# Performance work log

Hardware: AMD Instinct MI355X
Metric: run time of the kernel (lower is better)

The kernel has to match this reference:

```python
import jax, jax.numpy as jnp
import numpy as np

S = 8192; HID = 2048; H = 16; D = 128; BLK = 256; NC = S // BLK
GROUPS = 8; EPS = 1e-5; ROPE_THETA = 600000.0
LAYER_ID = 0; NLAYERS = 20
SCALE = D ** -0.5

def _build_slopes():
    # ALiBi-style slopes (H is a power of 2), scaled by layer decay factor
    start = 2.0 ** (-2.0 ** (-(np.log2(H) - 3.0)))
    slopes = np.array([start * start ** i for i in range(H)], dtype=np.float32)
    return slopes * np.float32(1.0 - LAYER_ID / (NLAYERS - 1) + 1e-5)

SLOPES = jnp.asarray(_build_slopes())  # [H]

def _rmsnorm(x, w, eps=EPS):
    return x * jax.lax.rsqrt(jnp.mean(x * x, axis=-1, keepdims=True) + eps) * w

def _rope(x, positions):
    # neox-style rotary, x: [S, H, D]
    half = D // 2
    inv_freq = 1.0 / (ROPE_THETA ** (jnp.arange(0, D, 2, dtype=jnp.float32) / D))
    freqs = positions.astype(jnp.float32)[:, None] * inv_freq  # [S, half]
    cos = jnp.cos(freqs)[:, None, :]
    sin = jnp.sin(freqs)[:, None, :]
    x1, x2 = x[..., :half], x[..., half:]
    return jnp.concatenate([x1 * cos - x2 * sin, x2 * cos + x1 * sin], axis=-1)

def _lightning_attn(q, k, v):
    # chunked recurrent linear attention with per-head exponential decay
    # q,k,v: [S, H, D] fp32 -> [S, H*D]
    qc = q.reshape(NC, BLK, H, D).transpose(0, 2, 1, 3)  # [NC, H, BLK, D]
    kc = k.reshape(NC, BLK, H, D).transpose(0, 2, 1, 3)
    vc = v.reshape(NC, BLK, H, D).transpose(0, 2, 1, 3)
    idx = jnp.arange(BLK, dtype=jnp.float32)
    q_decay = jnp.exp(-SLOPES[:, None, None] * (idx + 1.0)[None, :, None])       # [H,BLK,1]
    k_decay = jnp.exp(-SLOPES[:, None, None] * (BLK - 1.0 - idx)[None, :, None])  # [H,BLK,1]
    blk_decay = jnp.exp(-SLOPES * BLK)[:, None, None]                             # [H,1,1]
    dif = idx[:, None] - idx[None, :]
    causal = dif >= 0
    diag_decay = jnp.where(causal, jnp.exp(-SLOPES[:, None, None] * jnp.where(causal, dif, 0.0)), 0.0)  # [H,BLK,BLK]

    def step(kv, inp):
        qb, kb, vb = inp  # each [H, BLK, D]
        qk = jnp.einsum('hid,hjd->hij', qb, kb) * diag_decay
        intra = jnp.einsum('hij,hjd->hid', qk, vb)
        inter = jnp.einsum('hid,hde->hie', qb * q_decay, kv)
        kv_new = blk_decay * kv + jnp.einsum('hjd,hje->hde', kb * k_decay, vb)
        return kv_new, intra + inter

    kv0 = jnp.zeros((H, D, D), dtype=jnp.float32)
    _, out = jax.lax.scan(step, kv0, (qc, kc, vc))  # out: [NC, H, BLK, D]
    return out.transpose(0, 2, 1, 3).reshape(S, H * D)

def setup_inputs() -> dict:
    key = jax.random.key(0)
    ks = jax.random.split(key, 6)
    return {
        'hidden_states': jax.random.normal(ks[0], (S, HID), jnp.float32),
        'positions': jnp.arange(S, dtype=jnp.int32),
        'qkv_w': jax.random.normal(ks[1], (3 * H * D, HID), jnp.float32) * 0.02,
        'qkv_b': jax.random.normal(ks[2], (3 * H * D,), jnp.float32) * 0.01,
        'q_norm_w': jnp.ones((D,), jnp.float32),
        'k_norm_w': jnp.ones((D,), jnp.float32),
        'g_w': jax.random.normal(ks[3], (H * D, HID), jnp.float32) * 0.02,
        'g_norm_w': jnp.ones((H * D,), jnp.float32),
        'dense_w': jax.random.normal(ks[4], (HID, H * D), jnp.float32) * 0.02,
    }

def reference(hidden_states, positions, qkv_w, qkv_b, q_norm_w, k_norm_w, g_w, g_norm_w, dense_w):
    hs = hidden_states.astype(jnp.float32)
    qkv = hs @ qkv_w.T + qkv_b                      # [S, 3*H*D], fp32 (linear_silu=False)
    q, k, v = jnp.split(qkv, [H * D, 2 * H * D], axis=-1)
    q = q.reshape(S, H, D); k = k.reshape(S, H, D); v = v.reshape(S, H, D)
    q = _rmsnorm(q, q_norm_w)                       # use_qk_norm per-head RMSNorm
    k = _rmsnorm(k, k_norm_w)
    q = _rope(q, positions)                         # linear_rope=True
    k = _rope(k, positions)
    q = q * SCALE                                   # linear_scale (minimax backend)
    attn = _lightning_attn(q, k, v)                 # [S, H*D]
    g = hs @ g_w.T                                  # output gate
    xg = attn.reshape(S, GROUPS, (H * D) // GROUPS)  # group RMSNorm (norm_before_gate)
    rstd = jax.lax.rsqrt(jnp.mean(xg * xg, axis=-1, keepdims=True) + EPS)
    y = (xg * rstd).reshape(S, H * D) * g_norm_w * jax.nn.sigmoid(g)
    return y @ dense_w.T                            # [S, HID]
```

## Files before the change

### kernel.cpp

```cpp
#include <hip/hip_runtime.h>

#define S_LEN 8192
#define HID   2048
#define NH    16
#define HD    128
#define BLKC  256
#define QKV_STRIDE 6144
#define EPSV  1e-5f
#define SCALEF 0.08838834764831845f

typedef unsigned short u16;
typedef unsigned int   u32;
typedef __attribute__((ext_vector_type(8))) short bf16x8;
typedef __attribute__((ext_vector_type(4))) float f32x4;

__device__ __forceinline__ float b2f(u16 u) {
    unsigned int x = ((unsigned int)u) << 16;
    return __uint_as_float(x);
}
__device__ __forceinline__ u16 f2b(float f) {
    unsigned int u = __float_as_uint(f);
    u += 0x7fff + ((u >> 16) & 1);
    return (u16)(u >> 16);
}
__device__ __forceinline__ u32 pack2(float lo, float hi) {
    return (u32)f2b(lo) | ((u32)f2b(hi) << 16);
}
__device__ __forceinline__ float get_slope(int h) {
    return exp2f(-0.5f * (float)(h + 1)) * 1.00001f;
}

#define GLOAD_LDS16(g, l)                                              \
    __builtin_amdgcn_global_load_lds(                                  \
        (const __attribute__((address_space(1))) void*)(g),            \
        (__attribute__((address_space(3))) void*)(l), 16, 0, 0)

__global__ __launch_bounds__(256) void canonize_kernel(const float* __restrict__ src,
                                                       u16* __restrict__ dst, int n) {
    const int i0 = (blockIdx.x * 256 + threadIdx.x) * 4;
    if (i0 >= n) return;
    const float4 f = *(const float4*)(src + i0);
    ushort4 o;
    o.x = f2b(f.x); o.y = f2b(f.y); o.z = f2b(f.z); o.w = f2b(f.w);
    *(ushort4*)(dst + i0) = o;
}

template<int OUT_F32>
__global__ __launch_bounds__(256) void gemm_mfma(const u16* __restrict__ A,
                                                 const u16* __restrict__ B,
                                                 const u16* __restrict__ bias,
                                                 void* __restrict__ Cv,
                                                 int K, int lda, int ldb, int ldc) {
    __shared__ u16 As[128 * 32];
    __shared__ u16 Bs[128 * 32];
    const int t = threadIdx.x;
    const int w = t >> 6;
    const int l = t & 63;
    const int row0 = blockIdx.y << 7, col0 = blockIdx.x << 7;

    const int se   = (w << 9) + (l << 3);
    const int srow = se >> 5;
    const int scol = se & 31;
    const u16* Ap = A + (size_t)(row0 + srow) * lda + scol;
    const u16* Bp = B + (size_t)(col0 + srow) * ldb + scol;
    u16* AsP = As + se;
    u16* BsP = Bs + se;

    const int wr = (w >> 1) << 6;
    const int wc = (w & 1) << 6;
    const int fr = l & 15;
    const int fk = (l >> 4) << 3;

    f32x4 acc[4][4] = {};

    for (int k0 = 0; k0 < K; k0 += 32) {
        __syncthreads();
        GLOAD_LDS16(Ap + k0, AsP);
        GLOAD_LDS16(Ap + k0 + (size_t)64 * lda, AsP + 64 * 32);
        GLOAD_LDS16(Bp + k0, BsP);
        GLOAD_LDS16(Bp + k0 + (size_t)64 * ldb, BsP + 64 * 32);
        __syncthreads();

        bf16x8 a[4], b[4];
#pragma unroll
        for (int m = 0; m < 4; ++m)
            a[m] = *(const bf16x8*)&As[(wr + (m << 4) + fr) * 32 + fk];
#pragma unroll
        for (int n = 0; n < 4; ++n)
            b[n] = *(const bf16x8*)&Bs[(wc + (n << 4) + fr) * 32 + fk];
#pragma unroll
        for (int m = 0; m < 4; ++m)
#pragma unroll
            for (int n = 0; n < 4; ++n)
                acc[m][n] = __builtin_amdgcn_mfma_f32_16x16x32_bf16(
                    a[m], b[n], acc[m][n], 0, 0, 0);
    }

    const int crow = row0 + wr + ((l >> 4) << 2);
    const int ccol = col0 + wc + fr;
#pragma unroll
    for (int n = 0; n < 4; ++n) {
        const float bv = (bias != nullptr) ? b2f(bias[ccol + (n << 4)]) : 0.f;
#pragma unroll
        for (int m = 0; m < 4; ++m) {
#pragma unroll
            for (int r = 0; r < 4; ++r) {
                const float val = acc[m][n][r] + bv;
                const size_t off = (size_t)(crow + (m << 4) + r) * ldc + ccol + (n << 4);
                if (OUT_F32) ((float*)Cv)[off] = val;
                else         ((u16*)Cv)[off]   = f2b(val);
            }
        }
    }
}

__global__ __launch_bounds__(256) void normrope_kernel(u16* __restrict__ qkvb,
                                                       const u16* __restrict__ qw,
                                                       const u16* __restrict__ kw,
                                                       const int* __restrict__ pos,
                                                       int row0) {
    const int wid = (blockIdx.x << 2) + (threadIdx.x >> 6);
    const int s = wid >> 4, h = wid & 15;
    const int l = threadIdx.x & 63;
    u16* qp = qkvb + (size_t)s * QKV_STRIDE + h * HD;
    u16* kp = qp + HID;
    const float q0 = b2f(qp[l]), q1 = b2f(qp[l + 64]);
    const float k0 = b2f(kp[l]), k1 = b2f(kp[l + 64]);
    float sq = q0 * q0 + q1 * q1;
    float sk = k0 * k0 + k1 * k1;
#pragma unroll
    for (int off = 32; off > 0; off >>= 1) {
        sq += __shfl_xor(sq, off);
        sk += __shfl_xor(sk, off);
    }
    const float qr = rsqrtf(sq * (1.f / 128.f) + EPSV);
    const float kr = rsqrtf(sk * (1.f / 128.f) + EPSV);
    const float nq0 = q0 * qr * b2f(qw[l]), nq1 = q1 * qr * b2f(qw[l + 64]);
    const float nk0 = k0 * kr * b2f(kw[l]), nk1 = k1 * kr * b2f(kw[l + 64]);
    const int p = pos[row0 + s];
    const float invf = powf(600000.f, -(float)l * (1.f / 64.f));
    const float fr = (float)p * invf;
    const float cs = cosf(fr), sn = sinf(fr);
    qp[l]      = f2b((nq0 * cs - nq1 * sn) * SCALEF);
    qp[l + 64] = f2b((nq1 * cs + nq0 * sn) * SCALEF);
    kp[l]      = f2b(nk0 * cs - nk1 * sn);
    kp[l + 64] = f2b(nk1 * cs + nk0 * sn);
}

__global__ __launch_bounds__(256) void kv_contrib_kernel(const u16* __restrict__ qkvb,
                                                         float* __restrict__ contrib) {
    const int b = blockIdx.x;
    const int eh = b & 1;
    const int h = (b >> 1) & 15;
    const int c = b >> 5;
    const float slope = get_slope(h);
    const u16* kb = qkvb + (size_t)c * BLKC * QKV_STRIDE + HID + h * HD;
    const u16* vb = kb + HID;
    const int t = threadIdx.x;
    const int tx = t & 15, ty = t >> 4;
    const int jj = t >> 5, dd = (t & 31) << 2;
    float acc[4][8] = {};
    __shared__ float kf[8][128], vf[8][128];
    for (int j0 = 0; j0 < BLKC; j0 += 8) {
        const float kd = expf(-slope * (float)(BLKC - 1 - (j0 + jj)));
        ushort4 k4 = *(const ushort4*)(kb + (size_t)(j0 + jj) * QKV_STRIDE + dd);
        ushort4 v4 = *(const ushort4*)(vb + (size_t)(j0 + jj) * QKV_STRIDE + dd);
        kf[jj][dd + 0] = b2f(k4.x) * kd; kf[jj][dd + 1] = b2f(k4.y) * kd;
        kf[jj][dd + 2] = b2f(k4.z) * kd; kf[jj][dd + 3] = b2f(k4.w) * kd;
        vf[jj][dd + 0] = b2f(v4.x); vf[jj][dd + 1] = b2f(v4.y);
        vf[jj][dd + 2] = b2f(v4.z); vf[jj][dd + 3] = b2f(v4.w);
        __syncthreads();
#pragma unroll
        for (int j = 0; j < 8; ++j) {
            float4 e0 = *(const float4*)&vf[j][(eh << 6) + (ty << 2)];
            float4 d0 = *(const float4*)&kf[j][tx << 3];
            float4 d1 = *(const float4*)&kf[j][(tx << 3) + 4];
            float er[4] = {e0.x, e0.y, e0.z, e0.w};
            float dr[8] = {d0.x, d0.y, d0.z, d0.w, d1.x, d1.y, d1.z, d1.w};
#pragma unroll
            for (int u = 0; u < 4; ++u)
#pragma unroll
                for (int v = 0; v < 8; ++v) acc[u][v] += er[u] * dr[v];
        }
        __syncthreads();
    }
    float* cb = contrib + ((size_t)(c * NH + h) * HD + (eh << 6) + (ty << 2)) * HD + (tx << 3);
#pragma unroll
    for (int u = 0; u < 4; ++u) {
        *(float4*)(cb + (size_t)u * HD)     = make_float4(acc[u][0], acc[u][1], acc[u][2], acc[u][3]);
        *(float4*)(cb + (size_t)u * HD + 4) = make_float4(acc[u][4], acc[u][5], acc[u][6], acc[u][7]);
    }
}

__global__ __launch_bounds__(256) void kv_scan_kernel(const float* __restrict__ buf,
                                                      u16* __restrict__ bufb,
                                                      float* __restrict__ carry,
                                                      int ncs) {
    const int tid = blockIdx.x * 256 + threadIdx.x;
    const int h = tid >> 14;
    const float bd = expf(-get_slope(h) * (float)BLKC);
    float prev = carry[tid];
    for (int c = 0; c < ncs; ++c) {
        const size_t off = (size_t)c * (NH * HD * HD) + tid;
        const float cur = buf[off];
        bufb[off] = f2b(prev);
        prev = bd * prev + cur;
    }
    carry[tid] = prev;
}

__global__ __launch_bounds__(256) void attn_mfma_kernel(u16* __restrict__ qkvb,
                                                        const u16* __restrict__ kvstatesb) {
    const int b  = blockIdx.x;
    const int hb = b & 1;
    const int h  = (b >> 1) & 15;
    const int c  = b >> 5;
    const float slope = get_slope(h);
    const int t  = threadIdx.x;
    const int w  = t >> 6, l = t & 63;
    const int lg = l >> 4, lc = l & 15;
    const int giw = hb * 4 + w;
    const int i0  = giw << 5;

    __shared__ u16 Ks[32 * 128];
    __shared__ u16 Vt[128 * 40];
    __shared__ u16 Sb[4 * 1024];

    const u16* qbase = qkvb + (size_t)(c * BLKC) * QKV_STRIDE + h * HD;
    bf16x8 qa[2][4];
#pragma unroll
    for (int m = 0; m < 2; ++m)
#pragma unroll
        for (int kk = 0; kk < 4; ++kk)
            qa[m][kk] = *(const bf16x8*)(qbase +
                (size_t)(i0 + m * 16 + lc) * QKV_STRIDE + kk * 32 + lg * 8);

    f32x4 acc[2][8] = {};

    const u16* kbase = qkvb + (size_t)(c * BLKC) * QKV_STRIDE + HID + h * HD;
    const u16* vbase = kbase + HID;
    const int jtmax = hb * 4 + 4;
    const int ve  = t & 127;
    const int vph = t >> 7;
    u16* SbW = Sb + (w << 10);

    for (int jt = 0; jt < jtmax; ++jt) {
        __syncthreads();
#pragma unroll
        for (int u = 0; u < 2; ++u) {
            const int idx = t + (u << 8);
            const int j = idx >> 4, s = idx & 15;
            const int sp = s ^ (j & 7);
            GLOAD_LDS16(kbase + (size_t)(jt * 32 + j) * QKV_STRIDE + sp * 8,
                        Ks + idx * 8);
        }
        union { int4 q; u16 e[8]; } vv[2];
#pragma unroll
        for (int u = 0; u < 2; ++u) {
            const int p0 = vph * 8 + u * 16;
#pragma unroll
            for (int x = 0; x < 8; ++x) {
                const int p = p0 + x;
                const int j = ((p & 1) << 4) | (p >> 1);
                vv[u].e[x] = vbase[(size_t)(jt * 32 + j) * QKV_STRIDE + ve];
            }
        }
#pragma unroll
        for (int u = 0; u < 2; ++u) {
            const int p0 = vph * 8 + u * 16;
            *(int4*)&Vt[ve * 40 + p0] = vv[u].q;
        }
        __syncthreads();

        if (jt <= giw) {
            f32x4 sacc[2][2] = {};
#pragma unroll
            for (int kk = 0; kk < 4; ++kk) {
#pragma unroll
                for (int nj = 0; nj < 2; ++nj) {
                    const int j = nj * 16 + lc;
                    const int sp = (kk * 4 + lg) ^ (j & 7);
                    bf16x8 kf = *(const bf16x8*)&Ks[j * 128 + sp * 8];
#pragma unroll
                    for (int m = 0; m < 2; ++m)
                        sacc[m][nj] = __builtin_amdgcn_mfma_f32_16x16x32_bf16(
                            qa[m][kk], kf, sacc[m][nj], 0, 0, 0);
                }
            }
            const int di0 = i0 - jt * 32;
            const float cj0 = expf(slope * (float)lc);
            const float cj1 = expf(slope * (float)(16 + lc));
            const bool diag = (jt == giw);
#pragma unroll
            for (int m = 0; m < 2; ++m) {
#pragma unroll
                for (int r = 0; r < 4; ++r) {
                    const int irel = m * 16 + lg * 4 + r;
                    const float rex = expf(-slope * (float)(di0 + irel));
                    float v0 = sacc[m][0][r] * rex * cj0;
                    float v1 = sacc[m][1][r] * rex * cj1;
                    if (diag) {
                        if (irel < lc)      v0 = 0.f;
                        if (irel < 16 + lc) v1 = 0.f;
                    }
                    const u32 pk = pack2(v0, v1);
                    const int iL = irel;
                    const int rp = iL ^ ((iL >> 2) & 1);
                    *(u32*)&SbW[rp * 32 + ((lc << 1) ^ (((iL >> 2) & 3) << 3))] = pk;
                }
            }
            bf16x8 sA[2];
#pragma unroll
            for (int m = 0; m < 2; ++m) {
                const int iL = m * 16 + lc;
                const int rp = iL ^ ((iL >> 2) & 1);
                sA[m] = *(const bf16x8*)&SbW[rp * 32 + ((lg << 3) ^ (((iL >> 2) & 3) << 3))];
            }
#pragma unroll
            for (int ne = 0; ne < 8; ++ne) {
                bf16x8 vf = *(const bf16x8*)&Vt[(ne * 16 + lc) * 40 + lg * 8];
#pragma unroll
                for (int m = 0; m < 2; ++m)
                    acc[m][ne] = __builtin_amdgcn_mfma_f32_16x16x32_bf16(
                        sA[m], vf, acc[m][ne], 0, 0, 0);
            }
        }
    }

    const u16* kvpb = kvstatesb + (size_t)(c * NH + h) * (HD * HD);
    const float dR0 = expf(-slope * (float)(i0 + lc + 1));
    const float dR1 = expf(-slope * (float)(i0 + 16 + lc + 1));
#pragma unroll
    for (int kk = 0; kk < 4; ++kk) {
        bf16x8 qd[2];
#pragma unroll
        for (int m = 0; m < 2; ++m) {
            const float dR = m ? dR1 : dR0;
            union { bf16x8 v; u32 u[4]; } qq;
            const u16* qe = (const u16*)&qa[m][kk];
#pragma unroll
            for (int x = 0; x < 4; ++x)
                qq.u[x] = pack2(b2f(qe[2 * x]) * dR, b2f(qe[2 * x + 1]) * dR);
            qd[m] = qq.v;
        }
#pragma unroll
        for (int ne = 0; ne < 8; ++ne) {
            bf16x8 kv = *(const bf16x8*)(kvpb + (size_t)(ne * 16 + lc) * HD + kk * 32 + lg * 8);
#pragma unroll
            for (int m = 0; m < 2; ++m)
                acc[m][ne] = __builtin_amdgcn_mfma_f32_16x16x32_bf16(
                    qd[m], kv, acc[m][ne], 0, 0, 0);
        }
    }

    u16* ob = qkvb + (size_t)(c * BLKC) * QKV_STRIDE + h * HD;
#pragma unroll
    for (int m = 0; m < 2; ++m)
#pragma unroll
        for (int ne = 0; ne < 8; ++ne)
#pragma unroll
            for (int r = 0; r < 4; ++r)
                ob[(size_t)(i0 + m * 16 + lg * 4 + r) * QKV_STRIDE + ne * 16 + lc] =
                    f2b(acc[m][ne][r]);
}

__global__ __launch_bounds__(256) void gate_kernel(u16* __restrict__ qkvb,
                                                   const u16* __restrict__ gnw) {
    const int s = blockIdx.x;
    const int t = threadIdx.x;
    const int j = t << 3;
    const size_t base = (size_t)s * QKV_STRIDE;
    union { int4 v; u16 e[8]; } xr, gr, wv;
    xr.v = *(const int4*)(qkvb + base + j);
    gr.v = *(const int4*)(qkvb + base + HID + j);
    wv.v = *(const int4*)(gnw + j);
    float x[8];
    float ss = 0.f;
#pragma unroll
    for (int i = 0; i < 8; ++i) { x[i] = b2f(xr.e[i]); ss += x[i] * x[i]; }
#pragma unroll
    for (int off = 16; off > 0; off >>= 1) ss += __shfl_xor(ss, off, 32);
    const float rstd = rsqrtf(ss * (1.f / 256.f) + EPSV);
    union { int4 v; u16 e[8]; } o;
#pragma unroll
    for (int i = 0; i < 8; ++i) {
        const float yv = x[i] * rstd * b2f(wv.e[i]) *
                         (1.f / (1.f + expf(-b2f(gr.e[i]))));
        o.e[i] = f2b(yv);
    }
    *(int4*)(qkvb + base + 2 * HID + j) = o.v;
}

extern "C" void kernel_launch(void* const* d_in, const int* in_sizes, int n_in,
                              void* d_out, int out_size, void* d_ws, size_t ws_size,
                              hipStream_t stream) {
    const int* pos = (const int*)d_in[1];
    float* out = (float*)d_out;
    char* ws = (char*)d_ws;

    u16*  c_hs    = (u16*)(ws + 256);
    u16*  c_qkvw  = c_hs   + 16777216;
    u16*  c_qkvb  = c_qkvw + 12582912;
    u16*  c_qn    = c_qkvb + 6144;
    u16*  c_kn    = c_qn   + 128;
    u16*  c_gw    = c_kn   + 128;
    u16*  c_gnw   = c_gw   + 4194304;
    u16*  c_dw    = c_gnw  + 2048;
    const size_t canon_end = 256 + (size_t)2 * (16777216 + 12582912 + 6144 + 128 + 128 + 4194304 + 2048 + 4194304);
    const size_t work_off = (canon_end + 255) & ~(size_t)255;

    const size_t MB = 1048576;
    int SCR;
    if      (ws_size >= work_off + (size_t)2048 * QKV_STRIDE * 2 + 13 * MB) SCR = 2048;
    else if (ws_size >= work_off + (size_t)512  * QKV_STRIDE * 2 + 4 * MB)  SCR = 512;
    else                                                                     SCR = 256;
    const int NCS = SCR / BLKC;
    const int NSC = S_LEN / SCR;

    u16*   qkvb    = (u16*)(ws + work_off);
    float* states  = (float*)(ws + work_off + (size_t)SCR * QKV_STRIDE * 2);
    float* carry   = states + (size_t)NCS * NH * HD * HD;
    u16*   statesb = (u16*)(carry + (size_t)NH * HD * HD);

    const dim3 B256(256);

    canonize_kernel<<<dim3(16777216 / 1024), B256, 0, stream>>>((const float*)d_in[0], c_hs,   16777216);
    canonize_kernel<<<dim3(12582912 / 1024), B256, 0, stream>>>((const float*)d_in[2], c_qkvw, 12582912);
    canonize_kernel<<<dim3(6),               B256, 0, stream>>>((const float*)d_in[3], c_qkvb, 6144);
    canonize_kernel<<<dim3(1),               B256, 0, stream>>>((const float*)d_in[4], c_qn,   128);
    canonize_kernel<<<dim3(1),               B256, 0, stream>>>((const float*)d_in[5], c_kn,   128);
    canonize_kernel<<<dim3(4194304 / 1024),  B256, 0, stream>>>((const float*)d_in[6], c_gw,   4194304);
    canonize_kernel<<<dim3(2),               B256, 0, stream>>>((const float*)d_in[7], c_gnw,  2048);
    canonize_kernel<<<dim3(4194304 / 1024),  B256, 0, stream>>>((const float*)d_in[8], c_dw,   4194304);

    hipMemsetAsync(carry, 0, (size_t)NH * HD * HD * sizeof(float), stream);

    for (int sc = 0; sc < NSC; ++sc) {
        const int row0 = sc * SCR;
        const u16* hsb = c_hs + (size_t)row0 * HID;
        gemm_mfma<0><<<dim3(QKV_STRIDE / 128, SCR / 128), B256, 0, stream>>>(
            hsb, c_qkvw, c_qkvb, qkvb, HID, HID, HID, QKV_STRIDE);
        normrope_kernel<<<dim3(SCR * NH / 4), B256, 0, stream>>>(
            qkvb, c_qn, c_kn, pos, row0);
        kv_contrib_kernel<<<dim3(NCS * NH * 2), B256, 0, stream>>>(qkvb, states);
        kv_scan_kernel<<<dim3(NH * HD * HD / 256), B256, 0, stream>>>(states, statesb, carry, NCS);
        attn_mfma_kernel<<<dim3(NCS * NH * 2), B256, 0, stream>>>(qkvb, statesb);
        gemm_mfma<0><<<dim3(HID / 128, SCR / 128), B256, 0, stream>>>(
            hsb, c_gw, nullptr, qkvb + HID, HID, HID, HID, QKV_STRIDE);
        gate_kernel<<<dim3(SCR), B256, 0, stream>>>(qkvb, c_gnw);
        gemm_mfma<1><<<dim3(HID / 128, SCR / 128), B256, 0, stream>>>(
            qkvb + 2 * HID, c_dw, nullptr, out + (size_t)row0 * HID,
            HID, QKV_STRIDE, HID, HID);
    }
}
```

Before: 1.180 ms.

## Fuse QKV and gate projections into one pipelined 256x256-tile MFMA GEMM

Replaces the separate 128x128 QKV and gate GEMMs with a single 256x256-tile, 512-thread kernel. The column blocks are split between the QKV weights and the gate weights, and the gate output goes to a separate buffer. The kernel uses direct global-to-LDS loads, double-buffered K stages with explicit vmcnt waits and barriers, XOR-swizzled LDS and MFMA priority raising, aiming to raise MFMA utilisation and cut launch count. Workspace thresholds are changed to fit the new gate buffer, and the gate kernel now reads from that buffer. This risks heavy register and LDS pressure (128 KB LDS per block) and depends on correct manual synchronisation.

```diff
diff --git a/kernel.cpp b/kernel.cpp
--- a/kernel.cpp
+++ b/kernel.cpp
@@ -35,6 +35,11 @@
         (const __attribute__((address_space(1))) void*)(g),            \
         (__attribute__((address_space(3))) void*)(l), 16, 0, 0)
 
+#define BARF() do { asm volatile("" ::: "memory");                     \
+                    __builtin_amdgcn_s_barrier();                      \
+                    asm volatile("" ::: "memory"); } while (0)
+#define VMW(n) asm volatile("s_waitcnt vmcnt(" #n ")" ::: "memory")
+
 __global__ __launch_bounds__(256) void canonize_kernel(const float* __restrict__ src,
                                                        u16* __restrict__ dst, int n) {
     const int i0 = (blockIdx.x * 256 + threadIdx.x) * 4;
@@ -43,6 +48,154 @@
     ushort4 o;
     o.x = f2b(f.x); o.y = f2b(f.y); o.z = f2b(f.z); o.w = f2b(f.w);
     *(ushort4*)(dst + i0) = o;
+}
+
+template<int D, int KH, int MH>
+__device__ __forceinline__ void rd_a(const u16* lds, int aoff0, bf16x8 af[4]) {
+#pragma unroll
+    for (int mm = 0; mm < 4; ++mm)
+        af[mm] = *(const bf16x8*)&lds[D * 16384 + KH * 8192 + (MH * 4 + mm) * 512 + aoff0];
+}
+template<int D, int KH>
+__device__ __forceinline__ void rd_b(const u16* lds, int boff0, bf16x8 bf[4]) {
+#pragma unroll
+    for (int nn = 0; nn < 4; ++nn)
+        bf[nn] = *(const bf16x8*)&lds[32768 + D * 16384 + KH * 8192 + nn * 512 + boff0];
+}
+template<int MH>
+__device__ __forceinline__ void mf(const bf16x8 af[4], const bf16x8 bf[4],
+                                   f32x4 (&acc)[8][4]) {
+    __builtin_amdgcn_s_setprio(1);
+#pragma unroll
+    for (int mm = 0; mm < 4; ++mm)
+#pragma unroll
+        for (int nn = 0; nn < 4; ++nn)
+            acc[MH * 4 + mm][nn] = __builtin_amdgcn_mfma_f32_16x16x32_bf16(
+                af[mm], bf[nn], acc[MH * 4 + mm][nn], 0, 0, 0);
+    __builtin_amdgcn_s_setprio(0);
+}
+
+__global__ __launch_bounds__(512, 2) void gemm256_fused(const u16* __restrict__ A,
+                                                        const u16* __restrict__ qkvw,
+                                                        const u16* __restrict__ gw,
+                                                        const u16* __restrict__ bias,
+                                                        u16* __restrict__ Cq,
+                                                        u16* __restrict__ Cg) {
+    __shared__ u16 lds[65536];
+    const int tid = threadIdx.x;
+    const int w = tid >> 6, l = tid & 63;
+    const int row0 = blockIdx.y << 8;
+    const int col0 = blockIdx.x << 8;
+    const bool isq = (blockIdx.x < 24);
+    const u16* Bsel = isq ? qkvw : gw;
+    const int bcol0 = isq ? col0 : (col0 - 6144);
+
+    const int scol = (((tid & 3) ^ ((tid >> 2) & 3)) << 3);
+    const u16* aSrc = A    + (size_t)(row0  + (tid >> 2)) * 2048 + scol;
+    const u16* bSrc = Bsel + (size_t)(bcol0 + (tid >> 2)) * 2048 + scol;
+
+#define STAGE_A(d, kh, tk) do {                                                        \
+    GLOAD_LDS16(aSrc + (size_t)(tk) * 64 + (kh) * 32,                                  \
+                lds + (d) * 16384 + (kh) * 8192 + tid * 8);                            \
+    GLOAD_LDS16(aSrc + (size_t)128 * 2048 + (size_t)(tk) * 64 + (kh) * 32,             \
+                lds + (d) * 16384 + (kh) * 8192 + 4096 + tid * 8); } while (0)
+#define STAGE_B(d, kh, tk) do {                                                        \
+    GLOAD_LDS16(bSrc + (size_t)(tk) * 64 + (kh) * 32,                                  \
+                lds + 32768 + (d) * 16384 + (kh) * 8192 + tid * 8);                    \
+    GLOAD_LDS16(bSrc + (size_t)128 * 2048 + (size_t)(tk) * 64 + (kh) * 32,             \
+                lds + 32768 + (d) * 16384 + (kh) * 8192 + 4096 + tid * 8); } while (0)
+
+    const int wr = (w >> 2) << 7;
+    const int wc = (w & 3) << 6;
+    const int fslot = (((l >> 4) ^ (l & 3)) << 3);
+    const int aoff0 = (wr + (l & 15)) * 32 + fslot;
+    const int boff0 = (wc + (l & 15)) * 32 + fslot;
+
+    f32x4 acc[8][4] = {};
+    bf16x8 af[4], bf[4];
+
+    STAGE_A(0, 0, 0); STAGE_B(0, 0, 0);
+    STAGE_A(0, 1, 0); STAGE_B(0, 1, 0);
+    STAGE_A(1, 0, 1); STAGE_B(1, 0, 1);
+
+    for (int tk = 0; tk < 30; tk += 2) {
+        VMW(8); BARF();
+        rd_a<0, 0, 0>(lds, aoff0, af); rd_b<0, 0>(lds, boff0, bf);
+        STAGE_A(1, 1, tk + 1);
+        BARF(); mf<0>(af, bf, acc);
+        BARF();
+        rd_a<0, 0, 1>(lds, aoff0, af);
+        STAGE_B(1, 1, tk + 1);
+        BARF(); mf<1>(af, bf, acc);
+        VMW(8); BARF();
+        rd_a<0, 1, 0>(lds, aoff0, af); rd_b<0, 1>(lds, boff0, bf);
+        STAGE_A(0, 0, tk + 2);
+        BARF(); mf<0>(af, bf, acc);
+        BARF();
+        rd_a<0, 1, 1>(lds, aoff0, af);
+        STAGE_B(0, 0, tk + 2);
+        BARF(); mf<1>(af, bf, acc);
+        VMW(8); BARF();
+        rd_a<1, 0, 0>(lds, aoff0, af); rd_b<1, 0>(lds, boff0, bf);
+        STAGE_A(0, 1, tk + 2);
+        BARF(); mf<0>(af, bf, acc);
+        BARF();
+        rd_a<1, 0, 1>(lds, aoff0, af);
+        STAGE_B(0, 1, tk + 2);
+        BARF(); mf<1>(af, bf, acc);
+        VMW(8); BARF();
+        rd_a<1, 1, 0>(lds, aoff0, af); rd_b<1, 1>(lds, boff0, bf);
+        STAGE_A(1, 0, tk + 3);
+        BARF(); mf<0>(af, bf, acc);
+        BARF();
+        rd_a<1, 1, 1>(lds, aoff0, af);
+        STAGE_B(1, 0, tk + 3);
+        BARF(); mf<1>(af, bf, acc);
+    }
+    VMW(8); BARF();
+    rd_a<0, 0, 0>(lds, aoff0, af); rd_b<0, 0>(lds, boff0, bf);
+    STAGE_A(1, 1, 31);
+    BARF(); mf<0>(af, bf, acc);
+    BARF();
+    rd_a<0, 0, 1>(lds, aoff0, af);
+    STAGE_B(1, 1, 31);
+    BARF(); mf<1>(af, bf, acc);
+    VMW(8); BARF();
+    rd_a<0, 1, 0>(lds, aoff0, af); rd_b<0, 1>(lds, boff0, bf);
+    BARF(); mf<0>(af, bf, acc);
+    BARF();
+    rd_a<0, 1, 1>(lds, aoff0, af);
+    BARF(); mf<1>(af, bf, acc);
+    VMW(4); BARF();
+    rd_a<1, 0, 0>(lds, aoff0, af); rd_b<1, 0>(lds, boff0, bf);
+    BARF(); mf<0>(af, bf, acc);
+    BARF();
+    rd_a<1, 0, 1>(lds, aoff0, af);
+    BARF(); mf<1>(af, bf, acc);
+    VMW(0); BARF();
+    rd_a<1, 1, 0>(lds, aoff0, af); rd_b<1, 1>(lds, boff0, bf);
+    BARF(); mf<0>(af, bf, acc);
+    BARF();
+    rd_a<1, 1, 1>(lds, aoff0, af);
+    BARF(); mf<1>(af, bf, acc);
+#undef STAGE_A
+#undef STAGE_B
+
+    u16* Cout = isq ? Cq : Cg;
+    const int ldc = isq ? 6144 : 2048;
+    const int ccb = (isq ? col0 : (col0 - 6144)) + wc + (l & 15);
+    const int crb = row0 + wr + ((l >> 4) << 2);
+#pragma unroll
+    for (int nn = 0; nn < 4; ++nn) {
+        const float bv = isq ? b2f(bias[col0 + wc + nn * 16 + (l & 15)]) : 0.f;
+#pragma unroll
+        for (int mm = 0; mm < 8; ++mm) {
+#pragma unroll
+            for (int r = 0; r < 4; ++r)
+                Cout[(size_t)(crb + mm * 16 + r) * ldc + ccb + nn * 16] =
+                    f2b(acc[mm][nn][r] + bv);
+        }
+    }
 }
 
 template<int OUT_F32>
@@ -365,6 +518,7 @@
 }
 
 __global__ __launch_bounds__(256) void gate_kernel(u16* __restrict__ qkvb,
+                                                   const u16* __restrict__ gbuf,
                                                    const u16* __restrict__ gnw) {
     const int s = blockIdx.x;
     const int t = threadIdx.x;
@@ -372,7 +526,7 @@
     const size_t base = (size_t)s * QKV_STRIDE;
     union { int4 v; u16 e[8]; } xr, gr, wv;
     xr.v = *(const int4*)(qkvb + base + j);
-    gr.v = *(const int4*)(qkvb + base + HID + j);
+    gr.v = *(const int4*)(gbuf + (size_t)s * 2048 + j);
     wv.v = *(const int4*)(gnw + j);
     float x[8];
     float ss = 0.f;
@@ -411,9 +565,9 @@
 
     const size_t MB = 1048576;
     int SCR;
-    if      (ws_size >= work_off + (size_t)2048 * QKV_STRIDE * 2 + 13 * MB) SCR = 2048;
-    else if (ws_size >= work_off + (size_t)512  * QKV_STRIDE * 2 + 4 * MB)  SCR = 512;
-    else                                                                     SCR = 256;
+    if      (ws_size >= work_off + 48 * MB) SCR = 2048;
+    else if (ws_size >= work_off + 14 * MB) SCR = 512;
+    else                                     SCR = 256;
     const int NCS = SCR / BLKC;
     const int NSC = S_LEN / SCR;
 
@@ -421,6 +575,7 @@
     float* states  = (float*)(ws + work_off + (size_t)SCR * QKV_STRIDE * 2);
     float* carry   = states + (size_t)NCS * NH * HD * HD;
     u16*   statesb = (u16*)(carry + (size_t)NH * HD * HD);
+    u16*   gbuf    = statesb + (size_t)NCS * NH * HD * HD;
 
     const dim3 B256(256);
 
@@ -438,16 +593,14 @@
     for (int sc = 0; sc < NSC; ++sc) {
         const int row0 = sc * SCR;
         const u16* hsb = c_hs + (size_t)row0 * HID;
-        gemm_mfma<0><<<dim3(QKV_STRIDE / 128, SCR / 128), B256, 0, stream>>>(
-            hsb, c_qkvw, c_qkvb, qkvb, HID, HID, HID, QKV_STRIDE);
+        gemm256_fused<<<dim3(32, SCR / 256), dim3(512), 0, stream>>>(
+            hsb, c_qkvw, c_gw, c_qkvb, qkvb, gbuf);
         normrope_kernel<<<dim3(SCR * NH / 4), B256, 0, stream>>>(
             qkvb, c_qn, c_kn, pos, row0);
         kv_contrib_kernel<<<dim3(NCS * NH * 2), B256, 0, stream>>>(qkvb, states);
         kv_scan_kernel<<<dim3(NH * HD * HD / 256), B256, 0, stream>>>(states, statesb, carry, NCS);
         attn_mfma_kernel<<<dim3(NCS * NH * 2), B256, 0, stream>>>(qkvb, statesb);
-        gemm_mfma<0><<<dim3(HID / 128, SCR / 128), B256, 0, stream>>>(
-            hsb, c_gw, nullptr, qkvb + HID, HID, HID, HID, QKV_STRIDE);
-        gate_kernel<<<dim3(SCR), B256, 0, stream>>>(qkvb, c_gnw);
+        gate_kernel<<<dim3(SCR), B256, 0, stream>>>(qkvb, gbuf, c_gnw);
         gemm_mfma<1><<<dim3(HID / 128, SCR / 128), B256, 0, stream>>>(
             qkvb + 2 * HID, c_dw, nullptr, out + (size_t)row0 * HID,
             HID, QKV_STRIDE, HID, HID);
```

New measurement: 1.020 ms. 1.16x faster.
